# Kernel optimization log

Measured on AMD Instinct MI355X. Metric: run time of the kernel, lower is better.

## Reference

```python
import jax, jax.numpy as jnp
import numpy as np

N_NODES = 100000
N_EDGES = 1600000
N_GRAPHS = 128
NHID = 128
NLAYER = 4
BN_EPS = 1e-5


def setup_inputs() -> dict:
    key = jax.random.key(0)
    ks = jax.random.split(key, 12)
    x_idx = jax.random.randint(ks[0], (N_NODES,), 0, 100)
    edge_index = jax.random.randint(ks[1], (2, N_EDGES), 0, N_NODES)
    edge_attr = jax.random.randint(ks[2], (N_EDGES,), 0, 20)
    batch = jnp.sort(jax.random.randint(ks[3], (N_NODES,), 0, N_GRAPHS))
    s = 0.1
    return {
        "x_idx": x_idx,
        "edge_index": edge_index,
        "edge_attr": edge_attr,
        "batch": batch,
        "node_emb": jax.random.normal(ks[4], (100, NHID), jnp.float32) * s,
        "edge_emb": jax.random.normal(ks[5], (NLAYER, 20, NHID), jnp.float32) * s,
        "conv_w1": jax.random.normal(ks[6], (NLAYER, NHID, NHID), jnp.float32) * s,
        "conv_w2": jax.random.normal(ks[7], (NLAYER, NHID, NHID), jnp.float32) * s,
        "bn_gamma": jnp.ones((NLAYER, NHID), jnp.float32),
        "bn_beta": jnp.zeros((NLAYER, NHID), jnp.float32),
        "out_w1": jax.random.normal(ks[8], (NHID, NHID), jnp.float32) * s,
        "out_b1": jnp.zeros((NHID,), jnp.float32),
        "out_bn_gamma": jnp.ones((NHID,), jnp.float32),
        "out_bn_beta": jnp.zeros((NHID,), jnp.float32),
        "out_w2": jax.random.normal(ks[9], (NHID, 1), jnp.float32) * s,
        "out_b2": jnp.zeros((1,), jnp.float32),
    }


def _batchnorm(h, gamma, beta):
    mu = h.mean(axis=0)
    var = h.var(axis=0)
    return (h - mu) * jax.lax.rsqrt(var + BN_EPS) * gamma + beta


def reference(x_idx, edge_index, edge_attr, batch, node_emb, edge_emb,
              conv_w1, conv_w2, bn_gamma, bn_beta,
              out_w1, out_b1, out_bn_gamma, out_bn_beta, out_w2, out_b2):
    # input encoder: discrete embedding lookup  [N, nhid]
    x = node_emb[x_idx]
    src, dst = edge_index[0], edge_index[1]
    prev = x
    for l in range(NLAYER):
        ea = edge_emb[l][edge_attr]                      # [E, nhid] edge encoder
        msg = jax.nn.relu(x[src] + ea)                   # GINE messages
        agg = jax.ops.segment_sum(msg, dst, num_segments=N_NODES)
        h = x + agg                                      # (1+eps)*x + agg, eps=0
        h = jax.nn.relu(h @ conv_w1[l]) @ conv_w2[l]     # GINE nn (bias=False)
        h = _batchnorm(h, bn_gamma[l], bn_beta[l])
        h = jax.nn.relu(h)                               # dropout p=0 is a no-op
        h = h + prev                                     # residual
        prev = h
        x = h
    # add pooling over graphs
    g = jax.ops.segment_sum(x, batch, num_segments=N_GRAPHS)   # [B, nhid]
    # output encoder: Linear -> BN -> ReLU -> Linear
    o = g @ out_w1 + out_b1
    o = jax.nn.relu(_batchnorm(o, out_bn_gamma, out_bn_beta))
    o = o @ out_w2 + out_b2
    return o
```

## Files before the change

### kernel.cpp

```cpp
#include <hip/hip_runtime.h>

#define N_NODES 100000
#define N_EDGES 1600000
#define N_GRAPHS 128
#define NHID 128
#define NLAYER 4
#define BN_EPS 1e-5f

#define SCAN_ITEMS 1024
#define SCAN_NB ((N_NODES + SCAN_ITEMS - 1) / SCAN_ITEMS)

__device__ __forceinline__ float4 ld4(const float* p){ return *(const float4*)p; }
__device__ __forceinline__ void st4(float* p, float4 v){ *(float4*)p = v; }

typedef __attribute__((ext_vector_type(8))) short short8v;
typedef __attribute__((ext_vector_type(4))) float f32x4;

__device__ __forceinline__ void bsplit(float a, unsigned short& h, unsigned short& l){
    unsigned ab = __float_as_uint(a);
    h = (unsigned short)(ab >> 16);
    float hf = __uint_as_float((unsigned)h << 16);
    l = (unsigned short)(__float_as_uint(a - hf) >> 16);
}

__device__ __forceinline__ unsigned short brne(float a){
    unsigned ab = __float_as_uint(a);
    return (unsigned short)((ab + 0x7FFFu + ((ab >> 16) & 1u)) >> 16);
}
__device__ __forceinline__ float b2f(unsigned short b){
    return __uint_as_float((unsigned)b << 16);
}


__global__ void k_hist(const int* __restrict__ dst, int* __restrict__ counts){
    int e = blockIdx.x * 256 + threadIdx.x;
    if (e < N_EDGES) atomicAdd(&counts[dst[e]], 1);
}

__global__ void k_scan_partial(const int* __restrict__ counts, int* __restrict__ partial){
    __shared__ int s[256];
    int t = threadIdx.x;
    int base = blockIdx.x * SCAN_ITEMS + t * 4;
    int v = 0;
    #pragma unroll
    for (int k = 0; k < 4; k++) if (base + k < N_NODES) v += counts[base + k];
    s[t] = v;
    __syncthreads();
    for (int o = 128; o > 0; o >>= 1){
        if (t < o) s[t] += s[t + o];
        __syncthreads();
    }
    if (t == 0) partial[blockIdx.x] = s[0];
}

__global__ void k_scan_top(int* __restrict__ partial, int nb, int* __restrict__ row_ptr){
    __shared__ int s[128];
    int t = threadIdx.x;
    int v = (t < nb) ? partial[t] : 0;
    s[t] = v;
    __syncthreads();
    for (int d = 1; d < 128; d <<= 1){
        int add = (t >= d) ? s[t - d] : 0;
        __syncthreads();
        s[t] += add;
        __syncthreads();
    }
    if (t < nb) partial[t] = s[t] - v;
    if (t == 0) row_ptr[N_NODES] = N_EDGES;
}

__global__ void k_scan_final(const int* __restrict__ counts, const int* __restrict__ partial,
                             int* __restrict__ row_ptr){
    __shared__ int s[256];
    int t = threadIdx.x;
    int base = blockIdx.x * SCAN_ITEMS + t * 4;
    int v[4]; int tsum = 0;
    #pragma unroll
    for (int k = 0; k < 4; k++){ v[k] = (base + k < N_NODES) ? counts[base + k] : 0; tsum += v[k]; }
    s[t] = tsum;
    __syncthreads();
    for (int d = 1; d < 256; d <<= 1){
        int add = (t >= d) ? s[t - d] : 0;
        __syncthreads();
        s[t] += add;
        __syncthreads();
    }
    int off = partial[blockIdx.x] + s[t] - tsum;
    #pragma unroll
    for (int k = 0; k < 4; k++){
        if (base + k < N_NODES) row_ptr[base + k] = off;
        off += v[k];
    }
}

__global__ void k_fill(const int* __restrict__ eidx, const int* __restrict__ eattr,
                       const int* __restrict__ x_idx,
                       int* __restrict__ cursor, unsigned* __restrict__ pack){
    int e = blockIdx.x * 256 + threadIdx.x;
    if (e >= N_EDGES) return;
    int d = eidx[N_EDGES + e];
    int s = eidx[e];
    int a = eattr[e];
    int xi = x_idx[s];
    int pos = atomicAdd(&cursor[d], 1);
    pack[pos] = (unsigned)s | ((unsigned)a << 17) | ((unsigned)xi << 22);
}


__global__ void k_combo(const float* __restrict__ node_emb, const float* __restrict__ edge_emb0,
                        float* __restrict__ combo){
    int i = blockIdx.x * 256 + threadIdx.x;
    if (i >= 2000 * NHID) return;
    int row = i >> 7, c = i & 127;
    int ni = row / 20, a = row - ni * 20;
    combo[i] = fmaxf(node_emb[ni * NHID + c] + edge_emb0[a * NHID + c], 0.f);
}


__global__ void k_wsplit(const float* __restrict__ w1, const float* __restrict__ w2,
                         unsigned short* __restrict__ wth, unsigned short* __restrict__ wtl){
    int i = blockIdx.x * 256 + threadIdx.x;
    int which = i >> 16;
    int m = (i >> 14) & 3;
    int r = i & 16383;
    int k = r >> 7, c = r & 127;
    float v = (which ? w2 : w1)[m * 16384 + k * 128 + c];
    unsigned short h, l;
    bsplit(v, h, l);
    int o = ((which * 4 + m) * 128 + c) * 128 + k;
    wth[o] = h; wtl[o] = l;
}


__global__ void k_initx(const int* __restrict__ x_idx, const float* __restrict__ node_emb,
                        float4* __restrict__ x4){
    int i = blockIdx.x * 256 + threadIdx.x;
    if (i >= N_NODES * 32) return;
    int n = i >> 5, c = i & 31;
    int id = x_idx[n];
    x4[i] = ((const float4*)node_emb)[id * 32 + c];
}


__global__ __launch_bounds__(256) void k_agg(const float* __restrict__ x,
                      const ushort2* __restrict__ xb,
                      const int* __restrict__ row_ptr,
                      const unsigned* __restrict__ pack, const float* __restrict__ emb_l,
                      float2* __restrict__ h0){
    int gid = blockIdx.x * 256 + threadIdx.x;
    int node = gid >> 6;
    int lane = threadIdx.x & 63;
    const float2* x2 = (const float2*)x;
    const float2* e2 = (const float2*)emb_l;
    float2 acc = x2[node * 64 + lane];
    int beg = row_ptr[node], end = row_ptr[node + 1];
    int i = beg;
    for (; i + 3 < end; i += 4){
        unsigned p0 = pack[i], p1 = pack[i+1], p2 = pack[i+2], p3 = pack[i+3];
        ushort2 g0 = xb[(p0 & 0x1FFFFu) * 64 + lane];
        ushort2 g1 = xb[(p1 & 0x1FFFFu) * 64 + lane];
        ushort2 g2 = xb[(p2 & 0x1FFFFu) * 64 + lane];
        ushort2 g3 = xb[(p3 & 0x1FFFFu) * 64 + lane];
        float2 b0 = e2[((p0 >> 17) & 31u) * 64 + lane];
        float2 b1 = e2[((p1 >> 17) & 31u) * 64 + lane];
        float2 b2 = e2[((p2 >> 17) & 31u) * 64 + lane];
        float2 b3 = e2[((p3 >> 17) & 31u) * 64 + lane];
        acc.x += (fmaxf(b2f(g0.x) + b0.x, 0.f) + fmaxf(b2f(g1.x) + b1.x, 0.f))
               + (fmaxf(b2f(g2.x) + b2.x, 0.f) + fmaxf(b2f(g3.x) + b3.x, 0.f));
        acc.y += (fmaxf(b2f(g0.y) + b0.y, 0.f) + fmaxf(b2f(g1.y) + b1.y, 0.f))
               + (fmaxf(b2f(g2.y) + b2.y, 0.f) + fmaxf(b2f(g3.y) + b3.y, 0.f));
    }
    for (; i < end; i++){
        unsigned p = pack[i];
        ushort2 g = xb[(p & 0x1FFFFu) * 64 + lane];
        float2 ev = e2[((p >> 17) & 31u) * 64 + lane];
        acc.x += fmaxf(b2f(g.x) + ev.x, 0.f);
        acc.y += fmaxf(b2f(g.y) + ev.y, 0.f);
    }
    h0[node * 64 + lane] = acc;
}


__global__ __launch_bounds__(256) void k_agg0(const float* __restrict__ x,
                      const int* __restrict__ row_ptr,
                      const unsigned* __restrict__ pack,
                      const float* __restrict__ combo,
                      float2* __restrict__ h0){
    int gid = blockIdx.x * 256 + threadIdx.x;
    int node = gid >> 6;
    int lane = threadIdx.x & 63;
    const float2* x2 = (const float2*)x;
    const float2* c2 = (const float2*)combo;
    float2 acc = x2[node * 64 + lane];
    int beg = row_ptr[node], end = row_ptr[node + 1];
    int i = beg;
    for (; i + 3 < end; i += 4){
        unsigned p0 = pack[i], p1 = pack[i+1], p2 = pack[i+2], p3 = pack[i+3];
        int ci0 = (int)((p0 >> 22) & 127u) * 20 + (int)((p0 >> 17) & 31u);
        int ci1 = (int)((p1 >> 22) & 127u) * 20 + (int)((p1 >> 17) & 31u);
        int ci2 = (int)((p2 >> 22) & 127u) * 20 + (int)((p2 >> 17) & 31u);
        int ci3 = (int)((p3 >> 22) & 127u) * 20 + (int)((p3 >> 17) & 31u);
        float2 m0 = c2[ci0 * 64 + lane];
        float2 m1 = c2[ci1 * 64 + lane];
        float2 m2 = c2[ci2 * 64 + lane];
        float2 m3 = c2[ci3 * 64 + lane];
        acc.x += (m0.x + m1.x) + (m2.x + m3.x);
        acc.y += (m0.y + m1.y) + (m2.y + m3.y);
    }
    for (; i < end; i++){
        unsigned p = pack[i];
        int ci = (int)((p >> 22) & 127u) * 20 + (int)((p >> 17) & 31u);
        float2 m = c2[ci * 64 + lane];
        acc.x += m.x;
        acc.y += m.y;
    }
    h0[node * 64 + lane] = acc;
}


template<int RELU_OUT, int DO_STATS>
__global__ __launch_bounds__(256) void k_mfma(const float* __restrict__ A,
                                              const unsigned short* __restrict__ Wth,
                                              const unsigned short* __restrict__ Wtl,
                                              float* __restrict__ out,
                                              float* __restrict__ stats_l){
    __shared__ unsigned short Ah[128][40], Al[128][40];
    __shared__ unsigned short Bh[128][40], Bl[128][40];
    const int tid = threadIdx.x;
    const int w = tid >> 6;
    const int l = tid & 63;
    const int lr = l & 15;
    const int lk = l >> 4;
    const int row0 = blockIdx.x * 128;

    f32x4 acc[2][8];
    #pragma unroll
    for (int m = 0; m < 2; m++)
        #pragma unroll
        for (int n = 0; n < 8; n++) acc[m][n] = (f32x4)(0.f);

    for (int kc = 0; kc < 4; kc++){
        __syncthreads();
        #pragma unroll
        for (int q = 0; q < 4; q++){
            int f = tid + 256 * q;
            int r = f >> 3, kq = f & 7;
            int gr = row0 + r;
            float4 v = make_float4(0.f, 0.f, 0.f, 0.f);
            if (gr < N_NODES) v = ld4(A + (size_t)gr * NHID + kc * 32 + kq * 4);
            unsigned short h0,l0,h1,l1,h2,l2,h3,l3;
            bsplit(v.x, h0, l0); bsplit(v.y, h1, l1);
            bsplit(v.z, h2, l2); bsplit(v.w, h3, l3);
            *(ushort4*)&Ah[r][kq * 4] = make_ushort4(h0, h1, h2, h3);
            *(ushort4*)&Al[r][kq * 4] = make_ushort4(l0, l1, l2, l3);
        }
        #pragma unroll
        for (int q = 0; q < 2; q++){
            int f = tid + 256 * q;
            int c = f >> 2, kq = f & 3;
            size_t gi = (size_t)c * 128 + kc * 32 + kq * 8;
            *(uint4*)&Bh[c][kq * 8] = *(const uint4*)(Wth + gi);
            *(uint4*)&Bl[c][kq * 8] = *(const uint4*)(Wtl + gi);
        }
        __syncthreads();
        short8v pah[2], pal[2];
        #pragma unroll
        for (int m = 0; m < 2; m++){
            pah[m] = *(const short8v*)&Ah[w * 32 + m * 16 + lr][lk * 8];
            pal[m] = *(const short8v*)&Al[w * 32 + m * 16 + lr][lk * 8];
        }
        #pragma unroll
        for (int n = 0; n < 8; n++){
            short8v pbh = *(const short8v*)&Bh[n * 16 + lr][lk * 8];
            short8v pbl = *(const short8v*)&Bl[n * 16 + lr][lk * 8];
            #pragma unroll
            for (int m = 0; m < 2; m++){
                acc[m][n] = __builtin_amdgcn_mfma_f32_16x16x32_bf16(pal[m], pbh, acc[m][n], 0, 0, 0);
                acc[m][n] = __builtin_amdgcn_mfma_f32_16x16x32_bf16(pah[m], pbl, acc[m][n], 0, 0, 0);
                acc[m][n] = __builtin_amdgcn_mfma_f32_16x16x32_bf16(pah[m], pbh, acc[m][n], 0, 0, 0);
            }
        }
    }

    if (RELU_OUT){
        #pragma unroll
        for (int m = 0; m < 2; m++)
            #pragma unroll
            for (int n = 0; n < 8; n++)
                #pragma unroll
                for (int j = 0; j < 4; j++) acc[m][n][j] = fmaxf(acc[m][n][j], 0.f);
    }
    #pragma unroll
    for (int m = 0; m < 2; m++)
        #pragma unroll
        for (int j = 0; j < 4; j++){
            int gr = row0 + w * 32 + m * 16 + lk * 4 + j;
            if (gr < N_NODES){
                #pragma unroll
                for (int n = 0; n < 8; n++)
                    out[(size_t)gr * NHID + n * 16 + lr] = acc[m][n][j];
            }
        }

    if (DO_STATS){
        __syncthreads();
        float* red  = (float*)&Ah[0][0];
        float* red2 = (float*)&Bh[0][0];
        #pragma unroll
        for (int n = 0; n < 8; n++){
            float s = 0.f, q = 0.f;
            #pragma unroll
            for (int m = 0; m < 2; m++)
                #pragma unroll
                for (int j = 0; j < 4; j++){ float v = acc[m][n][j]; s += v; q += v * v; }
            red [(w * 4 + lk) * 128 + n * 16 + lr] = s;
            red2[(w * 4 + lk) * 128 + n * 16 + lr] = q;
        }
        __syncthreads();
        if (tid < 128){
            float s = 0.f, q = 0.f;
            #pragma unroll
            for (int r2 = 0; r2 < 16; r2++){
                s += red[r2 * 128 + tid];
                q += red2[r2 * 128 + tid];
            }
            atomicAdd(&stats_l[tid], s);
            atomicAdd(&stats_l[128 + tid], q);
        }
    }
}


__global__ void k_norm(const float4* __restrict__ h2, float4* __restrict__ x,
                       ushort4* __restrict__ xb,
                       const float* __restrict__ stats_l,
                       const float* __restrict__ gamma, const float* __restrict__ beta){
    int i = blockIdx.x * 256 + threadIdx.x;
    if (i >= N_NODES * 32) return;
    int g = (i & 31);
    float4 sv = ((const float4*)stats_l)[g];
    float4 qv = ((const float4*)(stats_l + 128))[g];
    float4 gm = ((const float4*)gamma)[g];
    float4 bt = ((const float4*)beta)[g];
    float4 ca, cb;
    {
        float mu, var;
        mu = sv.x * (1.f / N_NODES); var = qv.x * (1.f / N_NODES) - mu * mu;
        ca.x = gm.x * rsqrtf(var + BN_EPS); cb.x = bt.x - mu * ca.x;
        mu = sv.y * (1.f / N_NODES); var = qv.y * (1.f / N_NODES) - mu * mu;
        ca.y = gm.y * rsqrtf(var + BN_EPS); cb.y = bt.y - mu * ca.y;
        mu = sv.z * (1.f / N_NODES); var = qv.z * (1.f / N_NODES) - mu * mu;
        ca.z = gm.z * rsqrtf(var + BN_EPS); cb.z = bt.z - mu * ca.z;
        mu = sv.w * (1.f / N_NODES); var = qv.w * (1.f / N_NODES) - mu * mu;
        ca.w = gm.w * rsqrtf(var + BN_EPS); cb.w = bt.w - mu * ca.w;
    }
    float4 h = h2[i];
    float4 xv = x[i];
    float4 r;
    r.x = fmaxf(fmaf(h.x, ca.x, cb.x), 0.f) + xv.x;
    r.y = fmaxf(fmaf(h.y, ca.y, cb.y), 0.f) + xv.y;
    r.z = fmaxf(fmaf(h.z, ca.z, cb.z), 0.f) + xv.z;
    r.w = fmaxf(fmaf(h.w, ca.w, cb.w), 0.f) + xv.w;
    x[i] = r;
    xb[i] = make_ushort4(brne(r.x), brne(r.y), brne(r.z), brne(r.w));
}


__global__ void k_pool(const float* __restrict__ x, const int* __restrict__ batch,
                       float* __restrict__ gbuf){
    int g = blockIdx.x;
    int lo = 0, hi = N_NODES;
    while (lo < hi){ int mid = (lo + hi) >> 1; if (batch[mid] < g) lo = mid + 1; else hi = mid; }
    int start = lo;
    hi = N_NODES;
    while (lo < hi){ int mid = (lo + hi) >> 1; if (batch[mid] < g + 1) lo = mid + 1; else hi = mid; }
    int end = lo;
    int c = threadIdx.x & 127;
    int half = threadIdx.x >> 7;
    float acc = 0.f;
    for (int n = start + half; n < end; n += 2) acc += x[n * NHID + c];
    __shared__ float s[256];
    s[threadIdx.x] = acc;
    __syncthreads();
    if (threadIdx.x < 128) gbuf[g * NHID + threadIdx.x] = s[threadIdx.x] + s[threadIdx.x + 128];
}


__global__ __launch_bounds__(128) void k_head1(const float* __restrict__ gbuf,
                                               const float* __restrict__ w1,
                                               const float* __restrict__ b1,
                                               float* __restrict__ o1){
    __shared__ float gs[128];
    int i = blockIdx.x;
    int j = threadIdx.x;
    gs[j] = gbuf[i * NHID + j];
    __syncthreads();
    float acc = 0.f;
    #pragma unroll 8
    for (int k = 0; k < 128; k++)
        acc = fmaf(gs[k], w1[k * NHID + j], acc);
    o1[i * NHID + j] = acc + b1[j];
}

__global__ __launch_bounds__(128) void k_head2(const float* __restrict__ o1,
                                               const float* __restrict__ gamma,
                                               const float* __restrict__ beta,
                                               const float* __restrict__ w2,
                                               const float* __restrict__ b2,
                                               float* __restrict__ out){
    __shared__ float s_o1[128][129];
    __shared__ float sa[128], sb[128];
    int t = threadIdx.x;
    float s = 0.f, q = 0.f;
    for (int r = 0; r < 128; r++){
        float v = o1[r * NHID + t];
        s_o1[r][t] = v;
        s += v; q += v * v;
    }
    float mu = s * (1.f / 128.f);
    float rs = rsqrtf(q * (1.f / 128.f) - mu * mu + BN_EPS);
    float a = gamma[t] * rs;
    sa[t] = a;
    sb[t] = beta[t] - mu * a;
    __syncthreads();
    float a2 = 0.f;
    #pragma unroll 8
    for (int j = 0; j < 128; j++){
        float v = fmaf(s_o1[t][j], sa[j], sb[j]);
        a2 += fmaxf(v, 0.f) * w2[j];
    }
    out[t] = a2 + b2[0];
}


extern "C" void kernel_launch(void* const* d_in, const int* in_sizes, int n_in,
                              void* d_out, int out_size, void* d_ws, size_t ws_size,
                              hipStream_t stream){
    const int*   x_idx    = (const int*)d_in[0];
    const int*   eidx     = (const int*)d_in[1];
    const int*   eattr    = (const int*)d_in[2];
    const int*   batch    = (const int*)d_in[3];
    const float* node_emb = (const float*)d_in[4];
    const float* edge_emb = (const float*)d_in[5];
    const float* conv_w1  = (const float*)d_in[6];
    const float* conv_w2  = (const float*)d_in[7];
    const float* bn_gamma = (const float*)d_in[8];
    const float* bn_beta  = (const float*)d_in[9];
    const float* out_w1   = (const float*)d_in[10];
    const float* out_b1   = (const float*)d_in[11];
    const float* out_bng  = (const float*)d_in[12];
    const float* out_bnb  = (const float*)d_in[13];
    const float* out_w2   = (const float*)d_in[14];
    const float* out_b2   = (const float*)d_in[15];
    float* out = (float*)d_out;

    char* base = (char*)d_ws;
    size_t off = 0;
    auto alloc = [&](size_t bytes) -> char* {
        char* r = base + off;
        off = (off + bytes + 255) & ~(size_t)255;
        return r;
    };
    float*          xbuf    = (float*)alloc((size_t)N_NODES * NHID * 4);
    float*          h0buf   = (float*)alloc((size_t)N_NODES * NHID * 4);
    unsigned short* xbf     = (unsigned short*)alloc((size_t)N_NODES * NHID * 2);
    int*            row_ptr = (int*)alloc((size_t)(N_NODES + 1) * 4);
    int*            cursor  = (int*)alloc((size_t)N_NODES * 4);
    int*            counts  = (int*)alloc((size_t)N_NODES * 4);
    int*            partial = (int*)alloc(512 * 4);
    unsigned*       pack    = (unsigned*)alloc((size_t)N_EDGES * 4);
    float*          combo   = (float*)alloc((size_t)2000 * NHID * 4);
    unsigned short* wth     = (unsigned short*)alloc((size_t)8 * 16384 * 2);
    unsigned short* wtl     = (unsigned short*)alloc((size_t)8 * 16384 * 2);
    float*          stats   = (float*)alloc(NLAYER * 256 * 4);
    float*          gbuf    = (float*)alloc((size_t)N_GRAPHS * NHID * 4);
    float*          o1buf   = (float*)alloc((size_t)N_GRAPHS * NHID * 4);
    (void)ws_size; (void)in_sizes; (void)n_in; (void)out_size;

    hipMemsetAsync(counts, 0, (size_t)N_NODES * 4, stream);
    hipMemsetAsync(stats, 0, NLAYER * 256 * 4, stream);

    k_hist<<<N_EDGES / 256, 256, 0, stream>>>(eidx + N_EDGES, counts);
    k_scan_partial<<<SCAN_NB, 256, 0, stream>>>(counts, partial);
    k_scan_top<<<1, 128, 0, stream>>>(partial, SCAN_NB, row_ptr);
    k_scan_final<<<SCAN_NB, 256, 0, stream>>>(counts, partial, row_ptr);
    hipMemcpyAsync(cursor, row_ptr, (size_t)N_NODES * 4, hipMemcpyDeviceToDevice, stream);
    k_fill<<<N_EDGES / 256, 256, 0, stream>>>(eidx, eattr, x_idx, cursor, pack);

    k_combo<<<(2000 * NHID) / 256, 256, 0, stream>>>(node_emb, edge_emb, combo);
    k_wsplit<<<131072 / 256, 256, 0, stream>>>(conv_w1, conv_w2, wth, wtl);
    k_initx<<<(N_NODES * 32) / 256, 256, 0, stream>>>(x_idx, node_emb, (float4*)xbuf);

    const int gemm_grid = (N_NODES + 127) / 128;
    for (int l = 0; l < NLAYER; l++){
        if (l == 0){
            k_agg0<<<(N_NODES * 64) / 256, 256, 0, stream>>>(
                xbuf, row_ptr, pack, combo, (float2*)h0buf);
        } else {
            k_agg<<<(N_NODES * 64) / 256, 256, 0, stream>>>(
                xbuf, (const ushort2*)xbf, row_ptr, pack,
                edge_emb + (size_t)l * 20 * NHID, (float2*)h0buf);
        }
        k_mfma<1, 0><<<gemm_grid, 256, 0, stream>>>(
            h0buf, wth + (size_t)l * 16384, wtl + (size_t)l * 16384, h0buf, nullptr);
        k_mfma<0, 1><<<gemm_grid, 256, 0, stream>>>(
            h0buf, wth + (size_t)(4 + l) * 16384, wtl + (size_t)(4 + l) * 16384,
            h0buf, stats + l * 256);
        k_norm<<<(N_NODES * 32) / 256, 256, 0, stream>>>(
            (const float4*)h0buf, (float4*)xbuf, (ushort4*)xbf, stats + l * 256,
            bn_gamma + l * NHID, bn_beta + l * NHID);
    }

    k_pool<<<N_GRAPHS, 256, 0, stream>>>(xbuf, batch, gbuf);
    k_head1<<<N_GRAPHS, 128, 0, stream>>>(gbuf, out_w1, out_b1, o1buf);
    k_head2<<<1, 128, 0, stream>>>(o1buf, out_bng, out_bnb, out_w2, out_b2, out);
}
```

Measured before the change: 1.158 ms.

## Replace scattered CSR fill with two-pass bucketed fill via shared-memory staging

The CSR fill that scattered each edge directly to its destination slot with a global atomic is replaced by two passes. The first pass bins each chunk of 8192 edges into buckets of 256 destination nodes in shared memory, then writes each bucket contiguously into a temporary buffer. The second pass scatters each bucket into the final pack array, so the atomics and writes stay within a small region. The aim is to localize random global atomics and writes, at the cost of an extra 12.8MB temporary buffer round trip, two extra launches and about 70KB of shared memory per block, which limits occupancy.

```diff
diff --git a/kernel.cpp b/kernel.cpp
--- a/kernel.cpp
+++ b/kernel.cpp
@@ -9,6 +9,9 @@
 
 #define SCAN_ITEMS 1024
 #define SCAN_NB ((N_NODES + SCAN_ITEMS - 1) / SCAN_ITEMS)
+
+#define FILL_CHUNK 8192
+#define FILL_NB ((N_NODES + 255) / 256)
 
 __device__ __forceinline__ float4 ld4(const float* p){ return *(const float4*)p; }
 __device__ __forceinline__ void st4(float* p, float4 v){ *(float4*)p = v; }
@@ -93,17 +96,66 @@
     }
 }
 
-__global__ void k_fill(const int* __restrict__ eidx, const int* __restrict__ eattr,
-                       const int* __restrict__ x_idx,
-                       int* __restrict__ cursor, unsigned* __restrict__ pack){
-    int e = blockIdx.x * 256 + threadIdx.x;
-    if (e >= N_EDGES) return;
-    int d = eidx[N_EDGES + e];
-    int s = eidx[e];
-    int a = eattr[e];
-    int xi = x_idx[s];
-    int pos = atomicAdd(&cursor[d], 1);
-    pack[pos] = (unsigned)s | ((unsigned)a << 17) | ((unsigned)xi << 22);
+__global__ void k_binit(const int* __restrict__ row_ptr, int* __restrict__ bcur){
+    int b = blockIdx.x * 256 + threadIdx.x;
+    if (b < FILL_NB) bcur[b] = row_ptr[b * 256];
+}
+
+__global__ __launch_bounds__(256) void k_fillA(const int* __restrict__ eidx,
+                        const int* __restrict__ eattr, const int* __restrict__ x_idx,
+                        int* __restrict__ bcur, uint2* __restrict__ tmp){
+    __shared__ int cnt[FILL_NB];
+    __shared__ int lstart[FILL_NB];
+    __shared__ int lcur[FILL_NB];
+    __shared__ int gbase[FILL_NB];
+    __shared__ uint2 stage[FILL_CHUNK];
+    int t = threadIdx.x;
+    int e0 = blockIdx.x * FILL_CHUNK;
+    int n = min(FILL_CHUNK, N_EDGES - e0);
+    for (int i = t; i < FILL_NB; i += 256) cnt[i] = 0;
+    __syncthreads();
+    for (int i = t; i < n; i += 256)
+        atomicAdd(&cnt[(unsigned)eidx[N_EDGES + e0 + i] >> 8], 1);
+    __syncthreads();
+    if (t == 0){
+        int run = 0;
+        for (int b = 0; b < FILL_NB; b++){ lstart[b] = run; run += cnt[b]; }
+    }
+    __syncthreads();
+    for (int i = t; i < FILL_NB; i += 256) lcur[i] = lstart[i];
+    __syncthreads();
+    for (int i = t; i < n; i += 256){
+        int e = e0 + i;
+        int d = eidx[N_EDGES + e];
+        int s = eidx[e];
+        int a = eattr[e];
+        int xi = x_idx[s];
+        unsigned w = (unsigned)s | ((unsigned)a << 17) | ((unsigned)xi << 22);
+        int pos = atomicAdd(&lcur[d >> 8], 1);
+        stage[pos] = make_uint2(w, (unsigned)d);
+    }
+    __syncthreads();
+    for (int b = t; b < FILL_NB; b += 256)
+        if (cnt[b] > 0) gbase[b] = atomicAdd(&bcur[b], cnt[b]);
+    __syncthreads();
+    for (int i = t; i < n; i += 256){
+        uint2 v = stage[i];
+        int b = (int)(v.y >> 8);
+        tmp[gbase[b] + (i - lstart[b])] = v;
+    }
+}
+
+__global__ __launch_bounds__(256) void k_fillB(const uint2* __restrict__ tmp,
+                        const int* __restrict__ row_ptr,
+                        int* __restrict__ cursor, unsigned* __restrict__ pack){
+    int b = blockIdx.x;
+    int start = row_ptr[b * 256];
+    int end   = row_ptr[min((b + 1) * 256, N_NODES)];
+    for (int p = start + (int)threadIdx.x; p < end; p += 256){
+        uint2 v = tmp[p];
+        int pos = atomicAdd(&cursor[v.y], 1);
+        pack[pos] = v.x;
+    }
 }
 
 
@@ -468,7 +520,9 @@
     int*            cursor  = (int*)alloc((size_t)N_NODES * 4);
     int*            counts  = (int*)alloc((size_t)N_NODES * 4);
     int*            partial = (int*)alloc(512 * 4);
+    int*            bcur    = (int*)alloc((size_t)FILL_NB * 4);
     unsigned*       pack    = (unsigned*)alloc((size_t)N_EDGES * 4);
+    uint2*          tmp     = (uint2*)alloc((size_t)N_EDGES * 8);
     float*          combo   = (float*)alloc((size_t)2000 * NHID * 4);
     unsigned short* wth     = (unsigned short*)alloc((size_t)8 * 16384 * 2);
     unsigned short* wtl     = (unsigned short*)alloc((size_t)8 * 16384 * 2);
@@ -485,7 +539,10 @@
     k_scan_top<<<1, 128, 0, stream>>>(partial, SCAN_NB, row_ptr);
     k_scan_final<<<SCAN_NB, 256, 0, stream>>>(counts, partial, row_ptr);
     hipMemcpyAsync(cursor, row_ptr, (size_t)N_NODES * 4, hipMemcpyDeviceToDevice, stream);
-    k_fill<<<N_EDGES / 256, 256, 0, stream>>>(eidx, eattr, x_idx, cursor, pack);
+    k_binit<<<(FILL_NB + 255) / 256, 256, 0, stream>>>(row_ptr, bcur);
+    k_fillA<<<(N_EDGES + FILL_CHUNK - 1) / FILL_CHUNK, 256, 0, stream>>>(
+        eidx, eattr, x_idx, bcur, tmp);
+    k_fillB<<<FILL_NB, 256, 0, stream>>>(tmp, row_ptr, cursor, pack);
 
     k_combo<<<(2000 * NHID) / 256, 256, 0, stream>>>(node_emb, edge_emb, combo);
     k_wsplit<<<131072 / 256, 256, 0, stream>>>(conv_w1, conv_w2, wth, wtl);
```

Result: faster. 1.103 ms (-4.8%).
